# Performance work log

Measured on AMD Instinct MI355X. Metric: run time of the kernel, lower is better.

The kernel has to match this reference:

```python
import jax, jax.numpy as jnp
import numpy as np

B, L, D, H, NL = 32, 200, 64, 2, 2
ITEM_NUM, TIME_SPAN = 50000, 365
NEG = float(-2**32 + 1)


def _ln(x, g, b, eps=1e-8):
    m = jnp.mean(x, -1, keepdims=True)
    v = jnp.mean((x - m) ** 2, -1, keepdims=True)
    return (x - m) / jnp.sqrt(v + eps) * g + b


def setup_inputs() -> dict:
    key = jax.random.key(0)
    ks = iter(jax.random.split(key, 32))
    f = lambda shape: jax.random.normal(next(ks), shape, jnp.float32) * 0.02
    item_emb = f((ITEM_NUM + 1, D)).at[0].set(0.0)  # padding_idx=0
    return dict(
        log_ids=jax.random.randint(next(ks), (B, L), 0, ITEM_NUM + 1),
        log_times=jax.random.randint(next(ks), (B, L), 0, 100_000_000),
        pos_ids=jax.random.randint(next(ks), (B, L), 1, ITEM_NUM + 1),
        neg_ids=jax.random.randint(next(ks), (B, L), 1, ITEM_NUM + 1),
        item_emb=item_emb,
        posK_emb=f((L, D)), posV_emb=f((L, D)),
        tK_emb=f((TIME_SPAN + 1, D)), tV_emb=f((TIME_SPAN + 1, D)),
        ln1_g=jnp.ones((NL, D)), ln1_b=jnp.zeros((NL, D)),
        Wq=f((NL, D, D)), bq=jnp.zeros((NL, D)),
        Wk=f((NL, D, D)), bk=jnp.zeros((NL, D)),
        Wv=f((NL, D, D)), bv=jnp.zeros((NL, D)),
        ln2_g=jnp.ones((NL, D)), ln2_b=jnp.zeros((NL, D)),
        W1=f((NL, D, D)), b1=jnp.zeros((NL, D)),
        W2=f((NL, D, D)), b2=jnp.zeros((NL, D)),
        lnf_g=jnp.ones((D,)), lnf_b=jnp.zeros((D,)),
    )


def _attention(xq, xkv, pad, cmask, tK, tV, pK, pV, Wq, bq, Wk, bk, Wv, bv):
    dh = D // H
    Q = xq @ Wq.T + bq
    K = xkv @ Wk.T + bk
    V = xkv @ Wv.T + bv
    heads = lambda t: t.reshape(B, L, H, dh).transpose(2, 0, 1, 3)  # [H,B,L,dh]
    Qh, Kh, Vh = heads(Q), heads(K), heads(V)
    pKh = pK.reshape(L, H, dh).transpose(1, 0, 2)  # [H,L,dh] (same for all b)
    pVh = pV.reshape(L, H, dh).transpose(1, 0, 2)
    tKh = tK.reshape(B, L, L, H, dh).transpose(3, 0, 1, 2, 4)  # [H,B,Lq,Lk,dh]
    tVh = tV.reshape(B, L, L, H, dh).transpose(3, 0, 1, 2, 4)
    s = jnp.einsum('hbqd,hbkd->hbqk', Qh, Kh)
    s = s + jnp.einsum('hbqd,hkd->hbqk', Qh, pKh)
    s = s + jnp.einsum('hbqkd,hbqd->hbqk', tKh, Qh)
    s = s / (dh ** 0.5)
    s = jnp.where(pad[None, :, :, None], NEG, s)  # padded query rows
    s = jnp.where(cmask[None, None, :, :], NEG, s)  # causal mask
    A = jax.nn.softmax(s, axis=-1)
    out = jnp.einsum('hbqk,hbkd->hbqd', A, Vh)
    out = out + jnp.einsum('hbqk,hkd->hbqd', A, pVh)
    out = out + jnp.einsum('hbqk,hbqkd->hbqd', A, tVh)
    return out.transpose(1, 2, 0, 3).reshape(B, L, D)


def reference(log_ids, log_times, pos_ids, neg_ids, item_emb, posK_emb, posV_emb,
              tK_emb, tV_emb, ln1_g, ln1_b, Wq, bq, Wk, bk, Wv, bv,
              ln2_g, ln2_b, W1, b1, W2, b2, lnf_g, lnf_b):
    # per-pair time-interval buckets (days, clipped to TIME_SPAN)
    dt = jnp.abs(log_times[:, :, None] - log_times[:, None, :]).astype(jnp.float32) / 86400.0
    tmat = jnp.minimum(dt, TIME_SPAN).astype(jnp.int32)
    tK = tK_emb[tmat]  # [B,L,L,D]
    tV = tV_emb[tmat]
    pad = (log_ids == 0)
    keep = (~pad)[:, :, None].astype(item_emb.dtype)
    cmask = ~jnp.tril(jnp.ones((L, L), dtype=bool))
    x = item_emb[log_ids] * (D ** 0.5) * keep
    for i in range(NL):
        q = _ln(x, ln1_g[i], ln1_b[i])
        mha = _attention(q, x, pad, cmask, tK, tV, posK_emb, posV_emb,
                         Wq[i], bq[i], Wk[i], bk[i], Wv[i], bv[i])
        x = q + mha
        x = _ln(x, ln2_g[i], ln2_b[i])
        x = x + (jax.nn.relu(x @ W1[i].T + b1[i]) @ W2[i].T + b2[i])  # 1x1 conv FFN
        x = x * keep
    feats = _ln(x, lnf_g, lnf_b)
    pos_logits = jnp.sum(feats * item_emb[pos_ids], -1)
    neg_logits = jnp.sum(feats * item_emb[neg_ids], -1)
    return pos_logits, neg_logits
```

## Files before the change

### kernel.cpp

```cpp
#include <hip/hip_runtime.h>
#include <math.h>

#define BB 32
#define LLEN 200
#define DD 64
#define HH 2
#define NLAYER 2
#define BLD (BB * LLEN * DD)
#define TSPAN1 366

__device__ inline float waveSum(float v) {
#pragma unroll
    for (int off = 32; off > 0; off >>= 1) v += __shfl_xor(v, off);
    return v;
}
__device__ inline float halfSum(float v) {
    v += __shfl_xor(v, 1);
    v += __shfl_xor(v, 2);
    v += __shfl_xor(v, 4);
    v += __shfl_xor(v, 8);
    v += __shfl_xor(v, 16);
    return v;
}
__device__ inline float halfMax(float v) {
    v = fmaxf(v, __shfl_xor(v, 1));
    v = fmaxf(v, __shfl_xor(v, 2));
    v = fmaxf(v, __shfl_xor(v, 4));
    v = fmaxf(v, __shfl_xor(v, 8));
    v = fmaxf(v, __shfl_xor(v, 16));
    return v;
}

__global__ void transpose_kernel(const float* __restrict__ Wq,
                                 const float* __restrict__ Wk,
                                 const float* __restrict__ Wv,
                                 const float* __restrict__ W1,
                                 const float* __restrict__ W2,
                                 const float* __restrict__ tK_emb,
                                 float* __restrict__ wt,
                                 float* __restrict__ tKT) {
    int m = blockIdx.x;
    if (m < 10) {
        const float* src;
        switch (m % 5) {
            case 0: src = Wq; break;
            case 1: src = Wk; break;
            case 2: src = Wv; break;
            case 3: src = W1; break;
            default: src = W2; break;
        }
        src += (m / 5) * DD * DD;
        float* dst = wt + m * DD * DD;
        for (int e = threadIdx.x; e < DD * DD; e += 256) {
            int d = e >> 6, j = e & 63;
            dst[j * DD + d] = src[e];
        }
    } else {
        for (int e = threadIdx.x; e < TSPAN1 * DD; e += 256) {
            int t = e >> 6, d = e & 63;
            tKT[d * TSPAN1 + t] = tK_emb[e];
        }
    }
}

__global__ void embed_kernel(const int* __restrict__ log_ids,
                             const float* __restrict__ item_emb,
                             float* __restrict__ x) {
    int tid = threadIdx.x;
    int row = blockIdx.x * 4 + (tid >> 6);
    int d = tid & 63;
    int id = log_ids[row];
    float v = item_emb[id * DD + d] * 8.0f;
    x[row * DD + d] = (id == 0) ? 0.0f : v;
}

__global__ void ln_qkv_kernel(const float* __restrict__ x,
                              const float* __restrict__ g,
                              const float* __restrict__ bln,
                              const float* __restrict__ WqT, const float* __restrict__ bq,
                              const float* __restrict__ WkT, const float* __restrict__ bk,
                              const float* __restrict__ WvT, const float* __restrict__ bv,
                              const float* __restrict__ posK,
                              const float* __restrict__ posV,
                              float* __restrict__ q,
                              float* __restrict__ Q, float* __restrict__ K,
                              float* __restrict__ V) {
    __shared__ float qs[4][DD], xs[4][DD];
    int tid = threadIdx.x;
    int wid = tid >> 6, d = tid & 63;
    int row = blockIdx.x * 4 + wid;
    int l = row % LLEN;
    float xv = x[row * DD + d];
    xs[wid][d] = xv;
    float m = waveSum(xv) * (1.0f / 64.0f);
    float c = xv - m;
    float var = waveSum(c * c) * (1.0f / 64.0f);
    float qv = (c / sqrtf(var + 1e-8f)) * g[d] + bln[d];
    qs[wid][d] = qv;
    q[row * DD + d] = qv;
    float aq = bq[d], ak = bk[d], av = bv[d];
#pragma unroll 8
    for (int j = 0; j < DD; ++j) {
        aq = fmaf(qs[wid][j], WqT[j * DD + d], aq);
        ak = fmaf(xs[wid][j], WkT[j * DD + d], ak);
        av = fmaf(xs[wid][j], WvT[j * DD + d], av);
    }
    Q[row * DD + d] = aq;
    K[row * DD + d] = ak + posK[l * DD + d];
    V[row * DD + d] = av + posV[l * DD + d];
}

__global__ void qt_kernel(const float* __restrict__ Q,
                          const float* __restrict__ tKT,
                          float* __restrict__ Qt_g) {
    __shared__ float Qs[8][DD];
    int tid = threadIdx.x;
    int base = blockIdx.x * 8;
    for (int e = tid; e < 8 * DD; e += 384)
        Qs[e >> 6][e & 63] = Q[(base + (e >> 6)) * DD + (e & 63)];
    __syncthreads();
    int t = tid;
    if (t < TSPAN1) {
        float accA[8] = {0, 0, 0, 0, 0, 0, 0, 0};
        float accB[8] = {0, 0, 0, 0, 0, 0, 0, 0};
        for (int d = 0; d < 32; ++d) {
            float v = tKT[d * TSPAN1 + t];
#pragma unroll
            for (int gg = 0; gg < 8; ++gg) accA[gg] = fmaf(v, Qs[gg][d], accA[gg]);
        }
        for (int d = 32; d < 64; ++d) {
            float v = tKT[d * TSPAN1 + t];
#pragma unroll
            for (int gg = 0; gg < 8; ++gg) accB[gg] = fmaf(v, Qs[gg][d], accB[gg]);
        }
#pragma unroll
        for (int gg = 0; gg < 8; ++gg) {
            Qt_g[(base + gg) * (2 * TSPAN1) + t] = accA[gg];
            Qt_g[(base + gg) * (2 * TSPAN1) + TSPAN1 + t] = accB[gg];
        }
    }
}

__global__ void attn_kernel(const float* __restrict__ Q,
                            const float* __restrict__ Keff,
                            const float* __restrict__ Veff,
                            const int* __restrict__ log_times,
                            const float* __restrict__ Qt_g,
                            const float* __restrict__ tV_emb,
                            float* __restrict__ out) {
    __shared__ int t_s[LLEN];
    __shared__ float sc[4][HH][LLEN];
    __shared__ unsigned short tm_s[4][LLEN];
    __shared__ float qt_s[4][2 * TSPAN1];

    int tid = threadIdx.x;
    int wid = tid >> 6;
    int lane = tid & 63;
    int bi = blockIdx.x / 50;
    int i = blockIdx.x % 50;
    int qi = (wid == 0) ? i : (wid == 1) ? (99 - i) : (wid == 2) ? (100 + i) : (199 - i);
    int row = bi * LLEN + qi;
    int len = qi + 1;

    if (tid < LLEN) t_s[tid] = log_times[bi * LLEN + tid];
    __syncthreads();

    const float* qtrow = Qt_g + row * (2 * TSPAN1);
    for (int e = lane; e < 2 * TSPAN1; e += 64) qt_s[wid][e] = qtrow[e];

    int tq = t_s[qi];
    for (int k = lane; k < len; k += 64) {
        int dt = tq - t_s[k];
        if (dt < 0) dt = -dt;
        float dtf = fminf((float)dt * (1.0f / 86400.0f), 365.0f);
        tm_s[wid][k] = (unsigned short)(int)dtf;
    }

    int h = lane >> 5;
    int l5 = lane & 31;
    int cch = l5 >> 2;
    int j = l5 & 3;
    float4 qv = ((const float4*)(Q + row * DD))[h * 8 + cch];
    const float4* K4 = (const float4*)(Keff + bi * LLEN * DD);
    const float scale = 0.17677669529663687f;

    for (int k0 = 0; k0 < len; k0 += 4) {
        int k = k0 + j;
        int kc = (k < len) ? k : (len - 1);
        int bucket = tm_s[wid][kc];
        float4 kv = K4[kc * 16 + h * 8 + cch];
        float p = qv.x * kv.x + qv.y * kv.y + qv.z * kv.z + qv.w * kv.w;
        p += __shfl_xor(p, 4);
        p += __shfl_xor(p, 8);
        p += __shfl_xor(p, 16);
        float s = (p + qt_s[wid][h * TSPAN1 + bucket]) * scale;
        if (cch == 0 && k < len) sc[wid][h][k] = s;
    }

    {
        int kl = l5;
        float m = -INFINITY;
        for (int k = kl; k < len; k += 32) m = fmaxf(m, sc[wid][h][k]);
        m = halfMax(m);
        float s = 0.0f;
        for (int k = kl; k < len; k += 32) {
            float e = expf(sc[wid][h][k] - m);
            sc[wid][h][k] = e;
            s += e;
        }
        s = halfSum(s);
        float inv = 1.0f / s;
        for (int k = kl; k < len; k += 32) sc[wid][h][k] *= inv;
    }

    const float* Vb = Veff + bi * LLEN * DD + lane;
    const float* tVl = tV_emb + lane;
    float acc0 = 0.0f, acc1 = 0.0f, acc2 = 0.0f, acc3 = 0.0f;
    int k = 0;
    for (; k + 4 <= len; k += 4) {
        int b0 = tm_s[wid][k + 0];
        int b1 = tm_s[wid][k + 1];
        int b2 = tm_s[wid][k + 2];
        int b3 = tm_s[wid][k + 3];
        float a0 = sc[wid][h][k + 0];
        float a1 = sc[wid][h][k + 1];
        float a2 = sc[wid][h][k + 2];
        float a3 = sc[wid][h][k + 3];
        acc0 = fmaf(a0, Vb[(k + 0) * DD] + tVl[b0 * DD], acc0);
        acc1 = fmaf(a1, Vb[(k + 1) * DD] + tVl[b1 * DD], acc1);
        acc2 = fmaf(a2, Vb[(k + 2) * DD] + tVl[b2 * DD], acc2);
        acc3 = fmaf(a3, Vb[(k + 3) * DD] + tVl[b3 * DD], acc3);
    }
    for (; k < len; ++k) {
        int b0 = tm_s[wid][k];
        acc0 = fmaf(sc[wid][h][k], Vb[k * DD] + tVl[b0 * DD], acc0);
    }
    out[row * DD + lane] = (acc0 + acc1) + (acc2 + acc3);
}

__global__ void addln_ffn_kernel(const float* __restrict__ qin,
                                 const float* __restrict__ att,
                                 const float* __restrict__ g,
                                 const float* __restrict__ bln,
                                 const float* __restrict__ W1T, const float* __restrict__ b1,
                                 const float* __restrict__ W2T, const float* __restrict__ b2,
                                 const int* __restrict__ log_ids,
                                 float* __restrict__ xout) {
    __shared__ float xs[4][DD], hs[4][DD];
    int tid = threadIdx.x;
    int wid = tid >> 6, d = tid & 63;
    int row = blockIdx.x * 4 + wid;
    float v = qin[row * DD + d] + att[row * DD + d];
    float m = waveSum(v) * (1.0f / 64.0f);
    float c = v - m;
    float var = waveSum(c * c) * (1.0f / 64.0f);
    float xv = (c / sqrtf(var + 1e-8f)) * g[d] + bln[d];
    xs[wid][d] = xv;
    float a = b1[d];
#pragma unroll 8
    for (int j = 0; j < DD; ++j) a = fmaf(xs[wid][j], W1T[j * DD + d], a);
    hs[wid][d] = fmaxf(a, 0.0f);
    float o = b2[d];
#pragma unroll 8
    for (int j = 0; j < DD; ++j) o = fmaf(hs[wid][j], W2T[j * DD + d], o);
    float res = xv + o;
    if (log_ids[row] == 0) res = 0.0f;
    xout[row * DD + d] = res;
}

__global__ void final_kernel(const float* __restrict__ x,
                             const float* __restrict__ g,
                             const float* __restrict__ b,
                             const float* __restrict__ item_emb,
                             const int* __restrict__ pos_ids,
                             const int* __restrict__ neg_ids,
                             float* __restrict__ out) {
    int tid = threadIdx.x;
    int wid = tid >> 6, d = tid & 63;
    int row = blockIdx.x * 4 + wid;
    float v = x[row * DD + d];
    float m = waveSum(v) * (1.0f / 64.0f);
    float c = v - m;
    float var = waveSum(c * c) * (1.0f / 64.0f);
    float f = (c / sqrtf(var + 1e-8f)) * g[d] + b[d];
    int pid = pos_ids[row];
    int nid = neg_ids[row];
    float p = waveSum(f * item_emb[pid * DD + d]);
    float n = waveSum(f * item_emb[nid * DD + d]);
    if (d == 0) {
        out[row] = p;
        out[BB * LLEN + row] = n;
    }
}

extern "C" void kernel_launch(void* const* d_in, const int* in_sizes, int n_in,
                              void* d_out, int out_size, void* d_ws, size_t ws_size,
                              hipStream_t stream) {
    const int* log_ids = (const int*)d_in[0];
    const int* log_times = (const int*)d_in[1];
    const int* pos_ids = (const int*)d_in[2];
    const int* neg_ids = (const int*)d_in[3];
    const float* item_emb = (const float*)d_in[4];
    const float* posK = (const float*)d_in[5];
    const float* posV = (const float*)d_in[6];
    const float* tK_emb = (const float*)d_in[7];
    const float* tV_emb = (const float*)d_in[8];
    const float* ln1_g = (const float*)d_in[9];
    const float* ln1_b = (const float*)d_in[10];
    const float* Wq = (const float*)d_in[11];
    const float* bq = (const float*)d_in[12];
    const float* Wk = (const float*)d_in[13];
    const float* bk = (const float*)d_in[14];
    const float* Wv = (const float*)d_in[15];
    const float* bv = (const float*)d_in[16];
    const float* ln2_g = (const float*)d_in[17];
    const float* ln2_b = (const float*)d_in[18];
    const float* W1 = (const float*)d_in[19];
    const float* b1 = (const float*)d_in[20];
    const float* W2 = (const float*)d_in[21];
    const float* b2 = (const float*)d_in[22];
    const float* lnf_g = (const float*)d_in[23];
    const float* lnf_b = (const float*)d_in[24];

    float* ws = (float*)d_ws;
    float* x = ws;
    float* q = x + BLD;
    float* Qb = q + BLD;
    float* Kb = Qb + BLD;
    float* Vb = Kb + BLD;
    float* att = Vb + BLD;
    float* wt = att + BLD;
    float* tKT = wt + 10 * DD * DD;
    float* Qt = tKT + DD * TSPAN1;

    const int nrow = BB * LLEN;

    transpose_kernel<<<11, 256, 0, stream>>>(Wq, Wk, Wv, W1, W2, tK_emb, wt, tKT);
    embed_kernel<<<nrow / 4, 256, 0, stream>>>(log_ids, item_emb, x);

    for (int i = 0; i < NLAYER; ++i) {
        const float* WqT = wt + (i * 5 + 0) * DD * DD;
        const float* WkT = wt + (i * 5 + 1) * DD * DD;
        const float* WvT = wt + (i * 5 + 2) * DD * DD;
        const float* W1T = wt + (i * 5 + 3) * DD * DD;
        const float* W2T = wt + (i * 5 + 4) * DD * DD;
        ln_qkv_kernel<<<nrow / 4, 256, 0, stream>>>(x, ln1_g + i * DD, ln1_b + i * DD,
                                                    WqT, bq + i * DD,
                                                    WkT, bk + i * DD,
                                                    WvT, bv + i * DD,
                                                    posK, posV,
                                                    q, Qb, Kb, Vb);
        qt_kernel<<<nrow / 8, 384, 0, stream>>>(Qb, tKT, Qt);
        attn_kernel<<<BB * 50, 256, 0, stream>>>(Qb, Kb, Vb, log_times,
                                                 Qt, tV_emb, att);
        addln_ffn_kernel<<<nrow / 4, 256, 0, stream>>>(q, att, ln2_g + i * DD,
                                                       ln2_b + i * DD,
                                                       W1T, b1 + i * DD,
                                                       W2T, b2 + i * DD,
                                                       log_ids, x);
    }

    final_kernel<<<nrow / 4, 256, 0, stream>>>(x, lnf_g, lnf_b, item_emb,
                                               pos_ids, neg_ids, (float*)d_out);
}
```

Baseline: 196.9 us.

## Fuse embed, FFN, next-layer LN/QKV and final kernels; widen qt tile; drop qt smem staging

Folds the embedding lookup into the first LN/QKV kernel. Merges each layer's add+LN+FFN with the next layer's LN+QKV, or with the final LN and logit dot products, which cuts kernel launches and round trips of x through global memory. The qt kernel now processes 16 query rows per block instead of 8, reusing each tKT load across more FMAs. The attention kernel reads Qt entries directly from global memory instead of first staging the whole row in shared memory. Risks are higher register pressure in qt and scattered uncached global gathers in attention.

```diff
diff --git a/kernel.cpp b/kernel.cpp
--- a/kernel.cpp
+++ b/kernel.cpp
@@ -63,18 +63,8 @@
     }
 }
 
-__global__ void embed_kernel(const int* __restrict__ log_ids,
-                             const float* __restrict__ item_emb,
-                             float* __restrict__ x) {
-    int tid = threadIdx.x;
-    int row = blockIdx.x * 4 + (tid >> 6);
-    int d = tid & 63;
-    int id = log_ids[row];
-    float v = item_emb[id * DD + d] * 8.0f;
-    x[row * DD + d] = (id == 0) ? 0.0f : v;
-}
-
-__global__ void ln_qkv_kernel(const float* __restrict__ x,
+__global__ void ln_qkv_kernel(const int* __restrict__ log_ids,
+                              const float* __restrict__ item_emb,
                               const float* __restrict__ g,
                               const float* __restrict__ bln,
                               const float* __restrict__ WqT, const float* __restrict__ bq,
@@ -90,7 +80,8 @@
     int wid = tid >> 6, d = tid & 63;
     int row = blockIdx.x * 4 + wid;
     int l = row % LLEN;
-    float xv = x[row * DD + d];
+    int id = log_ids[row];
+    float xv = (id == 0) ? 0.0f : item_emb[id * DD + d] * 8.0f;
     xs[wid][d] = xv;
     float m = waveSum(xv) * (1.0f / 64.0f);
     float c = xv - m;
@@ -113,31 +104,35 @@
 __global__ void qt_kernel(const float* __restrict__ Q,
                           const float* __restrict__ tKT,
                           float* __restrict__ Qt_g) {
-    __shared__ float Qs[8][DD];
+    __shared__ float Qs[16][DD];
     int tid = threadIdx.x;
-    int base = blockIdx.x * 8;
-    for (int e = tid; e < 8 * DD; e += 384)
+    int base = blockIdx.x * 16;
+    for (int e = tid; e < 16 * DD; e += 384)
         Qs[e >> 6][e & 63] = Q[(base + (e >> 6)) * DD + (e & 63)];
     __syncthreads();
     int t = tid;
     if (t < TSPAN1) {
-        float accA[8] = {0, 0, 0, 0, 0, 0, 0, 0};
-        float accB[8] = {0, 0, 0, 0, 0, 0, 0, 0};
+        float acc[16];
+#pragma unroll
+        for (int gg = 0; gg < 16; ++gg) acc[gg] = 0.0f;
         for (int d = 0; d < 32; ++d) {
             float v = tKT[d * TSPAN1 + t];
 #pragma unroll
-            for (int gg = 0; gg < 8; ++gg) accA[gg] = fmaf(v, Qs[gg][d], accA[gg]);
-        }
+            for (int gg = 0; gg < 16; ++gg) acc[gg] = fmaf(v, Qs[gg][d], acc[gg]);
+        }
+#pragma unroll
+        for (int gg = 0; gg < 16; ++gg)
+            Qt_g[(base + gg) * (2 * TSPAN1) + t] = acc[gg];
+#pragma unroll
+        for (int gg = 0; gg < 16; ++gg) acc[gg] = 0.0f;
         for (int d = 32; d < 64; ++d) {
             float v = tKT[d * TSPAN1 + t];
 #pragma unroll
-            for (int gg = 0; gg < 8; ++gg) accB[gg] = fmaf(v, Qs[gg][d], accB[gg]);
-        }
-#pragma unroll
-        for (int gg = 0; gg < 8; ++gg) {
-            Qt_g[(base + gg) * (2 * TSPAN1) + t] = accA[gg];
-            Qt_g[(base + gg) * (2 * TSPAN1) + TSPAN1 + t] = accB[gg];
-        }
+            for (int gg = 0; gg < 16; ++gg) acc[gg] = fmaf(v, Qs[gg][d], acc[gg]);
+        }
+#pragma unroll
+        for (int gg = 0; gg < 16; ++gg)
+            Qt_g[(base + gg) * (2 * TSPAN1) + TSPAN1 + t] = acc[gg];
     }
 }
 
@@ -151,7 +146,6 @@
     __shared__ int t_s[LLEN];
     __shared__ float sc[4][HH][LLEN];
     __shared__ unsigned short tm_s[4][LLEN];
-    __shared__ float qt_s[4][2 * TSPAN1];
 
     int tid = threadIdx.x;
     int wid = tid >> 6;
@@ -165,9 +159,6 @@
     if (tid < LLEN) t_s[tid] = log_times[bi * LLEN + tid];
     __syncthreads();
 
-    const float* qtrow = Qt_g + row * (2 * TSPAN1);
-    for (int e = lane; e < 2 * TSPAN1; e += 64) qt_s[wid][e] = qtrow[e];
-
     int tq = t_s[qi];
     for (int k = lane; k < len; k += 64) {
         int dt = tq - t_s[k];
@@ -179,13 +170,14 @@
     int h = lane >> 5;
     int l5 = lane & 31;
     int cch = l5 >> 2;
-    int j = l5 & 3;
+    int jo = l5 & 3;
     float4 qv = ((const float4*)(Q + row * DD))[h * 8 + cch];
     const float4* K4 = (const float4*)(Keff + bi * LLEN * DD);
+    const float* qtrow = Qt_g + row * (2 * TSPAN1) + h * TSPAN1;
     const float scale = 0.17677669529663687f;
 
     for (int k0 = 0; k0 < len; k0 += 4) {
-        int k = k0 + j;
+        int k = k0 + jo;
         int kc = (k < len) ? k : (len - 1);
         int bucket = tm_s[wid][kc];
         float4 kv = K4[kc * 16 + h * 8 + cch];
@@ -193,24 +185,23 @@
         p += __shfl_xor(p, 4);
         p += __shfl_xor(p, 8);
         p += __shfl_xor(p, 16);
-        float s = (p + qt_s[wid][h * TSPAN1 + bucket]) * scale;
+        float s = (p + qtrow[bucket]) * scale;
         if (cch == 0 && k < len) sc[wid][h][k] = s;
     }
 
     {
-        int kl = l5;
         float m = -INFINITY;
-        for (int k = kl; k < len; k += 32) m = fmaxf(m, sc[wid][h][k]);
+        for (int k = l5; k < len; k += 32) m = fmaxf(m, sc[wid][h][k]);
         m = halfMax(m);
         float s = 0.0f;
-        for (int k = kl; k < len; k += 32) {
+        for (int k = l5; k < len; k += 32) {
             float e = expf(sc[wid][h][k] - m);
             sc[wid][h][k] = e;
             s += e;
         }
         s = halfSum(s);
         float inv = 1.0f / s;
-        for (int k = kl; k < len; k += 32) sc[wid][h][k] *= inv;
+        for (int k = l5; k < len; k += 32) sc[wid][h][k] *= inv;
     }
 
     const float* Vb = Veff + bi * LLEN * DD + lane;
@@ -238,14 +229,71 @@
     out[row * DD + lane] = (acc0 + acc1) + (acc2 + acc3);
 }
 
-__global__ void addln_ffn_kernel(const float* __restrict__ qin,
-                                 const float* __restrict__ att,
-                                 const float* __restrict__ g,
-                                 const float* __restrict__ bln,
-                                 const float* __restrict__ W1T, const float* __restrict__ b1,
-                                 const float* __restrict__ W2T, const float* __restrict__ b2,
-                                 const int* __restrict__ log_ids,
-                                 float* __restrict__ xout) {
+__global__ void mid_kernel(const float* __restrict__ qin,
+                           const float* __restrict__ att,
+                           const float* __restrict__ g2, const float* __restrict__ b2ln,
+                           const float* __restrict__ W1T, const float* __restrict__ b1v,
+                           const float* __restrict__ W2T, const float* __restrict__ b2v,
+                           const int* __restrict__ log_ids,
+                           const float* __restrict__ g1n, const float* __restrict__ b1n,
+                           const float* __restrict__ WqT, const float* __restrict__ bq,
+                           const float* __restrict__ WkT, const float* __restrict__ bk,
+                           const float* __restrict__ WvT, const float* __restrict__ bv,
+                           const float* __restrict__ posK,
+                           const float* __restrict__ posV,
+                           float* __restrict__ q,
+                           float* __restrict__ Q, float* __restrict__ K,
+                           float* __restrict__ V) {
+    __shared__ float xs[4][DD], hs[4][DD], qs[4][DD];
+    int tid = threadIdx.x;
+    int wid = tid >> 6, d = tid & 63;
+    int row = blockIdx.x * 4 + wid;
+    int l = row % LLEN;
+    float v = qin[row * DD + d] + att[row * DD + d];
+    float m = waveSum(v) * (1.0f / 64.0f);
+    float c = v - m;
+    float var = waveSum(c * c) * (1.0f / 64.0f);
+    float xv = (c / sqrtf(var + 1e-8f)) * g2[d] + b2ln[d];
+    xs[wid][d] = xv;
+    float a = b1v[d];
+#pragma unroll 8
+    for (int j = 0; j < DD; ++j) a = fmaf(xs[wid][j], W1T[j * DD + d], a);
+    hs[wid][d] = fmaxf(a, 0.0f);
+    float o = b2v[d];
+#pragma unroll 8
+    for (int j = 0; j < DD; ++j) o = fmaf(hs[wid][j], W2T[j * DD + d], o);
+    float res = xv + o;
+    if (log_ids[row] == 0) res = 0.0f;
+    float m2 = waveSum(res) * (1.0f / 64.0f);
+    float c2 = res - m2;
+    float var2 = waveSum(c2 * c2) * (1.0f / 64.0f);
+    float qv = (c2 / sqrtf(var2 + 1e-8f)) * g1n[d] + b1n[d];
+    qs[wid][d] = qv;
+    xs[wid][d] = res;
+    q[row * DD + d] = qv;
+    float aq = bq[d], ak = bk[d], av = bv[d];
+#pragma unroll 8
+    for (int j = 0; j < DD; ++j) {
+        aq = fmaf(qs[wid][j], WqT[j * DD + d], aq);
+        ak = fmaf(xs[wid][j], WkT[j * DD + d], ak);
+        av = fmaf(xs[wid][j], WvT[j * DD + d], av);
+    }
+    Q[row * DD + d] = aq;
+    K[row * DD + d] = ak + posK[l * DD + d];
+    V[row * DD + d] = av + posV[l * DD + d];
+}
+
+__global__ void end_kernel(const float* __restrict__ qin,
+                           const float* __restrict__ att,
+                           const float* __restrict__ g2, const float* __restrict__ b2ln,
+                           const float* __restrict__ W1T, const float* __restrict__ b1v,
+                           const float* __restrict__ W2T, const float* __restrict__ b2v,
+                           const int* __restrict__ log_ids,
+                           const float* __restrict__ lnf_g, const float* __restrict__ lnf_b,
+                           const float* __restrict__ item_emb,
+                           const int* __restrict__ pos_ids,
+                           const int* __restrict__ neg_ids,
+                           float* __restrict__ out) {
     __shared__ float xs[4][DD], hs[4][DD];
     int tid = threadIdx.x;
     int wid = tid >> 6, d = tid & 63;
@@ -254,35 +302,21 @@
     float m = waveSum(v) * (1.0f / 64.0f);
     float c = v - m;
     float var = waveSum(c * c) * (1.0f / 64.0f);
-    float xv = (c / sqrtf(var + 1e-8f)) * g[d] + bln[d];
+    float xv = (c / sqrtf(var + 1e-8f)) * g2[d] + b2ln[d];
     xs[wid][d] = xv;
-    float a = b1[d];
+    float a = b1v[d];
 #pragma unroll 8
     for (int j = 0; j < DD; ++j) a = fmaf(xs[wid][j], W1T[j * DD + d], a);
     hs[wid][d] = fmaxf(a, 0.0f);
-    float o = b2[d];
+    float o = b2v[d];
 #pragma unroll 8
     for (int j = 0; j < DD; ++j) o = fmaf(hs[wid][j], W2T[j * DD + d], o);
     float res = xv + o;
     if (log_ids[row] == 0) res = 0.0f;
-    xout[row * DD + d] = res;
-}
-
-__global__ void final_kernel(const float* __restrict__ x,
-                             const float* __restrict__ g,
-                             const float* __restrict__ b,
-                             const float* __restrict__ item_emb,
-                             const int* __restrict__ pos_ids,
-                             const int* __restrict__ neg_ids,
-                             float* __restrict__ out) {
-    int tid = threadIdx.x;
-    int wid = tid >> 6, d = tid & 63;
-    int row = blockIdx.x * 4 + wid;
-    float v = x[row * DD + d];
-    float m = waveSum(v) * (1.0f / 64.0f);
-    float c = v - m;
-    float var = waveSum(c * c) * (1.0f / 64.0f);
-    float f = (c / sqrtf(var + 1e-8f)) * g[d] + b[d];
+    float m2 = waveSum(res) * (1.0f / 64.0f);
+    float c2 = res - m2;
+    float var2 = waveSum(c2 * c2) * (1.0f / 64.0f);
+    float f = (c2 / sqrtf(var2 + 1e-8f)) * lnf_g[d] + lnf_b[d];
     int pid = pos_ids[row];
     int nid = neg_ids[row];
     float p = waveSum(f * item_emb[pid * DD + d]);
@@ -323,8 +357,7 @@
     const float* lnf_b = (const float*)d_in[24];
 
     float* ws = (float*)d_ws;
-    float* x = ws;
-    float* q = x + BLD;
+    float* q = ws;
     float* Qb = q + BLD;
     float* Kb = Qb + BLD;
     float* Vb = Kb + BLD;
@@ -335,31 +368,40 @@
 
     const int nrow = BB * LLEN;
 
+    const float* W1T0 = wt + 3 * DD * DD;
+    const float* W2T0 = wt + 4 * DD * DD;
+    const float* W1T1 = wt + 8 * DD * DD;
+    const float* W2T1 = wt + 9 * DD * DD;
+
     transpose_kernel<<<11, 256, 0, stream>>>(Wq, Wk, Wv, W1, W2, tK_emb, wt, tKT);
-    embed_kernel<<<nrow / 4, 256, 0, stream>>>(log_ids, item_emb, x);
-
-    for (int i = 0; i < NLAYER; ++i) {
-        const float* WqT = wt + (i * 5 + 0) * DD * DD;
-        const float* WkT = wt + (i * 5 + 1) * DD * DD;
-        const float* WvT = wt + (i * 5 + 2) * DD * DD;
-        const float* W1T = wt + (i * 5 + 3) * DD * DD;
-        const float* W2T = wt + (i * 5 + 4) * DD * DD;
-        ln_qkv_kernel<<<nrow / 4, 256, 0, stream>>>(x, ln1_g + i * DD, ln1_b + i * DD,
-                                                    WqT, bq + i * DD,
-                                                    WkT, bk + i * DD,
-                                                    WvT, bv + i * DD,
-                                                    posK, posV,
-                                                    q, Qb, Kb, Vb);
-        qt_kernel<<<nrow / 8, 384, 0, stream>>>(Qb, tKT, Qt);
-        attn_kernel<<<BB * 50, 256, 0, stream>>>(Qb, Kb, Vb, log_times,
-                                                 Qt, tV_emb, att);
-        addln_ffn_kernel<<<nrow / 4, 256, 0, stream>>>(q, att, ln2_g + i * DD,
-                                                       ln2_b + i * DD,
-                                                       W1T, b1 + i * DD,
-                                                       W2T, b2 + i * DD,
-                                                       log_ids, x);
-    }
-
-    final_kernel<<<nrow / 4, 256, 0, stream>>>(x, lnf_g, lnf_b, item_emb,
-                                               pos_ids, neg_ids, (float*)d_out);
-}
+
+    ln_qkv_kernel<<<nrow / 4, 256, 0, stream>>>(log_ids, item_emb,
+                                                ln1_g, ln1_b,
+                                                wt + 0 * DD * DD, bq,
+                                                wt + 1 * DD * DD, bk,
+                                                wt + 2 * DD * DD, bv,
+                                                posK, posV,
+                                                q, Qb, Kb, Vb);
+    qt_kernel<<<nrow / 16, 384, 0, stream>>>(Qb, tKT, Qt);
+    attn_kernel<<<BB * 50, 256, 0, stream>>>(Qb, Kb, Vb, log_times, Qt, tV_emb, att);
+
+    mid_kernel<<<nrow / 4, 256, 0, stream>>>(q, att,
+                                             ln2_g, ln2_b,
+                                             W1T0, b1, W2T0, b2,
+                                             log_ids,
+                                             ln1_g + DD, ln1_b + DD,
+                                             wt + 5 * DD * DD, bq + DD,
+                                             wt + 6 * DD * DD, bk + DD,
+                                             wt + 7 * DD * DD, bv + DD,
+                                             posK, posV,
+                                             q, Qb, Kb, Vb);
+    qt_kernel<<<nrow / 16, 384, 0, stream>>>(Qb, tKT, Qt);
+    attn_kernel<<<BB * 50, 256, 0, stream>>>(Qb, Kb, Vb, log_times, Qt, tV_emb, att);
+
+    end_kernel<<<nrow / 4, 256, 0, stream>>>(q, att,
+                                             ln2_g + DD, ln2_b + DD,
+                                             W1T1, b1 + DD, W2T1, b2 + DD,
+                                             log_ids,
+                                             lnf_g, lnf_b, item_emb,
+                                             pos_ids, neg_ids, (float*)d_out);
+}
```

Result: no change. 198.4 us (+0.7%).
